# Performance work log

Hardware: AMD Instinct MI355X
Metric: run time of the kernel (lower is better)

## Reference

```python
import jax, jax.numpy as jnp
import numpy as np

B, T, D, H = 32, 512, 512, 8
DH = D // H
NEG = -(2.0 ** 32) + 1.0  # matches torch's (-2**32 + 1) padding value
EPS = 1e-8


def setup_inputs() -> dict:
    key = jax.random.key(0)
    ks = jax.random.split(key, 10)
    s = 1.0 / np.sqrt(D)
    return {
        "queries": jax.random.normal(ks[0], (B, T, D), jnp.float32),
        "keys": jax.random.normal(ks[1], (B, T, D), jnp.float32),
        "Wq": jax.random.normal(ks[2], (D, D), jnp.float32) * s,
        "bq": jnp.zeros((D,), jnp.float32),
        "Wk": jax.random.normal(ks[3], (D, D), jnp.float32) * s,
        "bk": jnp.zeros((D,), jnp.float32),
        "Wv": jax.random.normal(ks[4], (D, D), jnp.float32) * s,
        "bv": jnp.zeros((D,), jnp.float32),
        "gamma": jnp.ones((D,), jnp.float32),
        "beta": jnp.zeros((D,), jnp.float32),
    }


def reference(queries, keys, Wq, bq, Wk, bk, Wv, bv, gamma, beta):
    b, tq, d = queries.shape
    tk = keys.shape[1]
    # projections (torch Linear: x @ W.T + b)
    Q = (queries @ Wq.T + bq).reshape(b, tq, H, DH)
    K = (keys @ Wk.T + bk).reshape(b, tk, H, DH)
    V = (keys @ Wv.T + bv).reshape(b, tk, H, DH)
    # scaled scores: [b, h, tq, tk]
    scores = jnp.einsum("bqhd,bkhd->bhqk", Q, K) / np.float32(np.sqrt(DH))
    # key padding mask (1 where key row sum != 0)
    key_mask = jnp.sign(jnp.abs(keys.sum(-1)))  # [b, tk]
    scores = jnp.where(key_mask[:, None, None, :] == 0, NEG, scores)
    # causal mask
    tril = jnp.tril(jnp.ones((tq, tk), scores.dtype))
    scores = jnp.where(tril[None, None, :, :] == 0, NEG, scores)
    attn = jax.nn.softmax(scores, axis=-1)  # [b, h, tq, tk]
    # query padding mask (zeros out rows for padded queries)
    query_mask = jnp.sign(jnp.abs(queries.sum(-1)))  # [b, tq]
    attn_m = attn * query_mask[:, None, :, None]
    # (dropout_rate == 0 -> identity)
    out = jnp.einsum("bhqk,bkhd->bqhd", attn_m, V).reshape(b, tq, d)
    # residual + LayerNorm (torch .std() is unbiased, ddof=1; eps added to std)
    x = out + queries
    mean = x.mean(-1, keepdims=True)
    std = jnp.std(x, axis=-1, ddof=1, keepdims=True)
    y = gamma * (x - mean) / (std + EPS) + beta
    return y
```

## Files before the change

### kernel.cpp

```cpp
#include <hip/hip_runtime.h>
#include <hip/hip_bf16.h>
#include <math.h>

#define B 32
#define T 512
#define D 512
#define H 8
#define DH 64
#define NEGV (-4294967295.0f)
#define LN_EPS 1e-8f

typedef __attribute__((ext_vector_type(8))) short bf16x8;
typedef __attribute__((ext_vector_type(4))) float f32x4;

__device__ inline f32x4 mfma16(bf16x8 a, bf16x8 b, f32x4 c) {
    return __builtin_amdgcn_mfma_f32_16x16x32_bf16(a, b, c, 0, 0, 0);
}

__device__ inline float fexp2(float x) { return __builtin_amdgcn_exp2f(x); }

#define GLDS16(g, l)                                                      \
    __builtin_amdgcn_global_load_lds(                                     \
        (const __attribute__((address_space(1))) void*)(g),               \
        (__attribute__((address_space(3))) void*)(l), 16, 0, 0)

__device__ inline unsigned short bf16bits(float x) {
    __hip_bfloat16 h = __float2bfloat16(x);
    union { __hip_bfloat16 h; unsigned short u; } cv;
    cv.h = h;
    return cv.u;
}

__global__ __launch_bounds__(256) void convert_mask(
    const float* __restrict__ queries, const float* __restrict__ keys,
    __hip_bfloat16* __restrict__ Qx, __hip_bfloat16* __restrict__ Kx,
    float* __restrict__ qmask, float* __restrict__ kmask)
{
    const int tid = threadIdx.x;
    const int wid = tid >> 6;
    const int lane = tid & 63;
    const int row = blockIdx.x * 4 + wid;
    const float* src = blockIdx.y ? keys : queries;
    __hip_bfloat16* dst = blockIdx.y ? Kx : Qx;
    float* dm = blockIdx.y ? kmask : qmask;

    const float4* p = (const float4*)(src + (size_t)row * 512);
    float4 a = p[lane * 2];
    float4 c = p[lane * 2 + 1];
    float s = a.x + a.y + a.z + a.w + c.x + c.y + c.z + c.w;

    union { unsigned short u[8]; bf16x8 v; } pk;
    pk.u[0] = bf16bits(a.x); pk.u[1] = bf16bits(a.y);
    pk.u[2] = bf16bits(a.z); pk.u[3] = bf16bits(a.w);
    pk.u[4] = bf16bits(c.x); pk.u[5] = bf16bits(c.y);
    pk.u[6] = bf16bits(c.z); pk.u[7] = bf16bits(c.w);
    *(bf16x8*)&dst[(size_t)row * 512 + lane * 8] = pk.v;

#pragma unroll
    for (int off = 32; off > 0; off >>= 1) s += __shfl_xor(s, off, 64);
    if (lane == 0) dm[row] = (s != 0.0f) ? 1.0f : 0.0f;
}

__global__ __launch_bounds__(256) void convert_w(
    const float* __restrict__ Wq, const float* __restrict__ Wk,
    const float* __restrict__ Wv, __hip_bfloat16* __restrict__ Wbf)
{
    const int mat = blockIdx.y;
    const float* Ws = (mat == 0) ? Wq : (mat == 1) ? Wk : Wv;
    const int i = (blockIdx.x * 256 + threadIdx.x) * 8;
    float4 a = *(const float4*)&Ws[i];
    float4 c = *(const float4*)&Ws[i + 4];
    union { unsigned short u[8]; bf16x8 v; } pk;
    pk.u[0] = bf16bits(a.x); pk.u[1] = bf16bits(a.y);
    pk.u[2] = bf16bits(a.z); pk.u[3] = bf16bits(a.w);
    pk.u[4] = bf16bits(c.x); pk.u[5] = bf16bits(c.y);
    pk.u[6] = bf16bits(c.z); pk.u[7] = bf16bits(c.w);
    *(bf16x8*)&Wbf[(size_t)mat * 262144 + i] = pk.v;
}

__global__ __launch_bounds__(256) void qkv_qk(
    const __hip_bfloat16* __restrict__ Qx, const __hip_bfloat16* __restrict__ Kx,
    const __hip_bfloat16* __restrict__ Wbf,
    const float* __restrict__ bq, const float* __restrict__ bk,
    __hip_bfloat16* __restrict__ Qbf, __hip_bfloat16* __restrict__ Kbf)
{
    const int mat = blockIdx.z;
    const __hip_bfloat16* X  = mat ? Kx : Qx;
    const __hip_bfloat16* Wm = Wbf + (size_t)mat * 262144;
    const float* bias = mat ? bk : bq;
    __hip_bfloat16* Out = mat ? Kbf : Qbf;
    const float sc = mat ? 1.0f : 0.18033688011112042f;

    const int bm = blockIdx.x * 128;
    const int bn = blockIdx.y * 128;
    const int tid = threadIdx.x;
    const int w = tid >> 6, lane = tid & 63;
    const int lo = lane & 15, hi = lane >> 4;
    const int wm = (w >> 1) * 64, wn = (w & 1) * 64;

    __shared__ __hip_bfloat16 As[2][128 * 32];
    __shared__ __hip_bfloat16 Bs[2][128 * 32];

    const int r0 = tid >> 2,          g0 = (tid & 3) ^ ((r0 >> 1) & 3);
    const int r1 = (tid + 256) >> 2,  g1 = ((tid + 256) & 3) ^ ((r1 >> 1) & 3);
    const __hip_bfloat16* sA0 = X  + (size_t)(bm + r0) * 512 + g0 * 8;
    const __hip_bfloat16* sA1 = X  + (size_t)(bm + r1) * 512 + g1 * 8;
    const __hip_bfloat16* sB0 = Wm + (size_t)(bn + r0) * 512 + g0 * 8;
    const __hip_bfloat16* sB1 = Wm + (size_t)(bn + r1) * 512 + g1 * 8;
    const int dst0 = (w * 64) * 8;
    const int dst1 = (256 + w * 64) * 8;

    int offA[4], offB[4];
#pragma unroll
    for (int mi = 0; mi < 4; ++mi) {
        int r = wm + mi * 16 + lo;
        offA[mi] = r * 32 + ((hi ^ ((r >> 1) & 3)) * 8);
    }
#pragma unroll
    for (int ni = 0; ni < 4; ++ni) {
        int r = wn + ni * 16 + lo;
        offB[ni] = r * 32 + ((hi ^ ((r >> 1) & 3)) * 8);
    }

    f32x4 acc[4][4];
#pragma unroll
    for (int mi = 0; mi < 4; ++mi)
#pragma unroll
        for (int ni = 0; ni < 4; ++ni)
            acc[mi][ni] = (f32x4){0.f, 0.f, 0.f, 0.f};

    GLDS16(sA0, &As[0][dst0]);
    GLDS16(sA1, &As[0][dst1]);
    GLDS16(sB0, &Bs[0][dst0]);
    GLDS16(sB1, &Bs[0][dst1]);
    __syncthreads();

    for (int kt = 0; kt < 16; ++kt) {
        const int cur = kt & 1;
        if (kt < 15) {
            const int k0 = (kt + 1) * 32;
            GLDS16(sA0 + k0, &As[cur ^ 1][dst0]);
            GLDS16(sA1 + k0, &As[cur ^ 1][dst1]);
            GLDS16(sB0 + k0, &Bs[cur ^ 1][dst0]);
            GLDS16(sB1 + k0, &Bs[cur ^ 1][dst1]);
        }
        bf16x8 af[4], bfr[4];
#pragma unroll
        for (int mi = 0; mi < 4; ++mi) af[mi]  = *(const bf16x8*)&As[cur][offA[mi]];
#pragma unroll
        for (int ni = 0; ni < 4; ++ni) bfr[ni] = *(const bf16x8*)&Bs[cur][offB[ni]];
#pragma unroll
        for (int mi = 0; mi < 4; ++mi)
#pragma unroll
            for (int ni = 0; ni < 4; ++ni)
                acc[mi][ni] = mfma16(bfr[ni], af[mi], acc[mi][ni]);
        __syncthreads();
    }

    float4 b4[4];
#pragma unroll
    for (int ni = 0; ni < 4; ++ni)
        b4[ni] = *(const float4*)&bias[bn + wn + ni * 16 + hi * 4];
#pragma unroll
    for (int mi = 0; mi < 4; ++mi) {
        const size_t tok = bm + wm + mi * 16 + lo;
        __hip_bfloat16* orow = Out + tok * 512 + bn + wn + hi * 4;
#pragma unroll
        for (int ni = 0; ni < 4; ++ni) {
            union { ushort4 u4; unsigned short us[4]; } pk;
            pk.us[0] = bf16bits((acc[mi][ni][0] + b4[ni].x) * sc);
            pk.us[1] = bf16bits((acc[mi][ni][1] + b4[ni].y) * sc);
            pk.us[2] = bf16bits((acc[mi][ni][2] + b4[ni].z) * sc);
            pk.us[3] = bf16bits((acc[mi][ni][3] + b4[ni].w) * sc);
            *(ushort4*)(orow + ni * 16) = pk.u4;
        }
    }
}

__global__ __launch_bounds__(256) void qkv_v(
    const __hip_bfloat16* __restrict__ Kx, const __hip_bfloat16* __restrict__ Wbf,
    const float* __restrict__ bv, __hip_bfloat16* __restrict__ Vtb)
{
    const __hip_bfloat16* X  = Kx;
    const __hip_bfloat16* Wm = Wbf + (size_t)2 * 262144;
    const float* bias = bv;

    const int bm = blockIdx.x * 128;
    const int bn = blockIdx.y * 128;
    const int tid = threadIdx.x;
    const int w = tid >> 6, lane = tid & 63;
    const int lo = lane & 15, hi = lane >> 4;
    const int wm = (w >> 1) * 64, wn = (w & 1) * 64;

    __shared__ __hip_bfloat16 As[2][128 * 32];
    __shared__ __hip_bfloat16 Bs[2][128 * 32];

    const int r0 = tid >> 2,          g0 = (tid & 3) ^ ((r0 >> 1) & 3);
    const int r1 = (tid + 256) >> 2,  g1 = ((tid + 256) & 3) ^ ((r1 >> 1) & 3);
    const __hip_bfloat16* sA0 = X  + (size_t)(bm + r0) * 512 + g0 * 8;
    const __hip_bfloat16* sA1 = X  + (size_t)(bm + r1) * 512 + g1 * 8;
    const __hip_bfloat16* sB0 = Wm + (size_t)(bn + r0) * 512 + g0 * 8;
    const __hip_bfloat16* sB1 = Wm + (size_t)(bn + r1) * 512 + g1 * 8;
    const int dst0 = (w * 64) * 8;
    const int dst1 = (256 + w * 64) * 8;

    int offA[4], offB[4];
#pragma unroll
    for (int mi = 0; mi < 4; ++mi) {
        int r = wm + mi * 16 + lo;
        offA[mi] = r * 32 + ((hi ^ ((r >> 1) & 3)) * 8);
    }
#pragma unroll
    for (int ni = 0; ni < 4; ++ni) {
        int r = wn + ni * 16 + lo;
        offB[ni] = r * 32 + ((hi ^ ((r >> 1) & 3)) * 8);
    }

    f32x4 acc[4][4];
#pragma unroll
    for (int mi = 0; mi < 4; ++mi)
#pragma unroll
        for (int ni = 0; ni < 4; ++ni)
            acc[mi][ni] = (f32x4){0.f, 0.f, 0.f, 0.f};

    GLDS16(sA0, &As[0][dst0]);
    GLDS16(sA1, &As[0][dst1]);
    GLDS16(sB0, &Bs[0][dst0]);
    GLDS16(sB1, &Bs[0][dst1]);
    __syncthreads();

    for (int kt = 0; kt < 16; ++kt) {
        const int cur = kt & 1;
        if (kt < 15) {
            const int k0 = (kt + 1) * 32;
            GLDS16(sA0 + k0, &As[cur ^ 1][dst0]);
            GLDS16(sA1 + k0, &As[cur ^ 1][dst1]);
            GLDS16(sB0 + k0, &Bs[cur ^ 1][dst0]);
            GLDS16(sB1 + k0, &Bs[cur ^ 1][dst1]);
        }
        bf16x8 af[4], bfr[4];
#pragma unroll
        for (int mi = 0; mi < 4; ++mi) af[mi]  = *(const bf16x8*)&As[cur][offA[mi]];
#pragma unroll
        for (int ni = 0; ni < 4; ++ni) bfr[ni] = *(const bf16x8*)&Bs[cur][offB[ni]];
#pragma unroll
        for (int mi = 0; mi < 4; ++mi)
#pragma unroll
            for (int ni = 0; ni < 4; ++ni)
                acc[mi][ni] = mfma16(af[mi], bfr[ni], acc[mi][ni]);
        __syncthreads();
    }

    float bcol[4];
#pragma unroll
    for (int ni = 0; ni < 4; ++ni) bcol[ni] = bias[bn + wn + ni * 16 + lo];
    const int bb = bm >> 9;
    const int tb = (bm & 511) + wm;
#pragma unroll
    for (int ni = 0; ni < 4; ++ni) {
        const int n = bn + wn + ni * 16 + lo;
        const int hh = n >> 6, dh = n & 63;
#pragma unroll
        for (int mi = 0; mi < 4; ++mi) {
            const int tok = tb + mi * 16 + hi * 4;
            const int ktl = tok >> 6, tl = tok & 63;
            union { ushort4 u4; unsigned short us[4]; } pk;
#pragma unroll
            for (int j = 0; j < 4; ++j)
                pk.us[j] = bf16bits(acc[mi][ni][j] + bcol[ni]);
            *(ushort4*)(Vtb + ((((size_t)(bb * 8 + hh) * 8 + ktl) * 64 + dh) * 64 + tl))
                = pk.u4;
        }
    }
}

__global__ __launch_bounds__(256, 4) void flash_attn(
    const __hip_bfloat16* __restrict__ Qbf, const __hip_bfloat16* __restrict__ Kbf,
    const __hip_bfloat16* __restrict__ Vtb, const float* __restrict__ qmask,
    const float* __restrict__ kmask, __hip_bfloat16* __restrict__ Oattn)
{
    const int flat = blockIdx.x + (blockIdx.y << 2) + (blockIdx.z << 5);
    const int rm = ((flat & 7) << 7) + (flat >> 3);
    const int pr = rm & 3;
    const int h  = (rm >> 2) & 7;
    const int b  = rm >> 5;

    const int tid  = threadIdx.x;
    const int w    = tid >> 6;
    const int lane = tid & 63;
    const int lo = lane & 15;
    const int hi = lane >> 4;

    __shared__ __hip_bfloat16 Ks[2][4096];
    __shared__ __hip_bfloat16 p_lds[4][16][72];

    const float* km = kmask + b * T;
    const __hip_bfloat16* Kh = Kbf + (size_t)b * T * D + h * DH;
    const __hip_bfloat16* Vh = Vtb + (size_t)(b * H + h) * T * DH;

    const int sr0 = tid >> 3,         ss0 = tid & 7,        sg0 = ss0 ^ (sr0 & 7);
    const int sr1 = (tid + 256) >> 3, ss1 = (tid + 256) & 7, sg1 = ss1 ^ (sr1 & 7);
    const __hip_bfloat16* sK0 = Kh + (size_t)sr0 * 512 + sg0 * 8;
    const __hip_bfloat16* sK1 = Kh + (size_t)sr1 * 512 + sg1 * 8;
    __hip_bfloat16* dK0a = &Ks[0][w * 512];
    __hip_bfloat16* dK0b = &Ks[0][2048 + w * 512];
    __hip_bfloat16* dK1a = &Ks[1][w * 512];
    __hip_bfloat16* dK1b = &Ks[1][2048 + w * 512];

#define STAGEK(bufp, kt) do {                                              \
        const size_t _o = (size_t)(kt) * 32768;                            \
        GLDS16(sK0 + _o, (bufp) ? dK1a : dK0a);                            \
        GLDS16(sK1 + _o, (bufp) ? dK1b : dK0b);                            \
    } while (0)

    int kfoff[4][2];
#pragma unroll
    for (int c = 0; c < 4; ++c)
#pragma unroll
        for (int j = 0; j < 2; ++j)
            kfoff[c][j] = (c * 16 + lo) * 64 + (((j * 4 + hi) ^ (lo & 7)) * 8);

    const int nt1 = pr + 1;

    int qtile = pr;
    int q = qtile * 64 + w * 16 + lo;
    const __hip_bfloat16* Qrow = Qbf + (size_t)(b * T + q) * D + h * DH;
    bf16x8 qf0 = *(const bf16x8*)(Qrow + hi * 8);
    bf16x8 qf1 = *(const bf16x8*)(Qrow + 32 + hi * 8);

    f32x4 o[4];
    float mrun = -INFINITY, lrun = 0.f;
#pragma unroll
    for (int d = 0; d < 4; ++d) o[d] = (f32x4){0.f, 0.f, 0.f, 0.f};

    STAGEK(0, 0);

    for (int i = 0; i < 9; ++i) {
        const int cur = i & 1;
        if (i < 8) {
            const int nxt = (i + 1 < nt1) ? (i + 1) : (i + 1 - nt1);
            STAGEK(cur ^ 1, nxt);
            asm volatile("s_waitcnt vmcnt(2)" ::: "memory");
        } else {
            asm volatile("s_waitcnt vmcnt(0)" ::: "memory");
        }
        __builtin_amdgcn_s_barrier();
        __builtin_amdgcn_sched_barrier(0);

        if (i == nt1) {
            const float inv = qmask[b * T + q] / lrun;
            __hip_bfloat16* orow = Oattn + (size_t)(b * T + q) * D + h * DH;
#pragma unroll
            for (int db = 0; db < 4; ++db) {
                union { ushort4 u4; unsigned short us[4]; } pk;
#pragma unroll
                for (int j = 0; j < 4; ++j)
                    pk.us[j] = bf16bits(o[db][j] * inv);
                *(ushort4*)(orow + db * 16 + hi * 4) = pk.u4;
            }
            qtile = 7 - pr;
            q = qtile * 64 + w * 16 + lo;
            const __hip_bfloat16* Qrow2 = Qbf + (size_t)(b * T + q) * D + h * DH;
            qf0 = *(const bf16x8*)(Qrow2 + hi * 8);
            qf1 = *(const bf16x8*)(Qrow2 + 32 + hi * 8);
            mrun = -INFINITY; lrun = 0.f;
#pragma unroll
            for (int d = 0; d < 4; ++d) o[d] = (f32x4){0.f, 0.f, 0.f, 0.f};
        }

        const int kt = (i < nt1) ? i : (i - nt1);
        const int kb = kt * 64;

        const __hip_bfloat16* Vtile = Vh + (size_t)kt * 4096;
        bf16x8 vf[4][2];
#pragma unroll
        for (int db = 0; db < 4; ++db) {
            const __hip_bfloat16* Vrow = Vtile + (db * 16 + lo) * 64;
            vf[db][0] = *(const bf16x8*)(Vrow + hi * 8);
            vf[db][1] = *(const bf16x8*)(Vrow + 32 + hi * 8);
        }

        bf16x8 kf[4][2];
#pragma unroll
        for (int c = 0; c < 4; ++c) {
            kf[c][0] = *(const bf16x8*)&Ks[cur][kfoff[c][0]];
            kf[c][1] = *(const bf16x8*)&Ks[cur][kfoff[c][1]];
        }

        f32x4 S[4];
#pragma unroll
        for (int c = 0; c < 4; ++c) {
            f32x4 acc = (f32x4){0.f, 0.f, 0.f, 0.f};
            acc = mfma16(kf[c][0], qf0, acc);
            acc = mfma16(kf[c][1], qf1, acc);
            const float4 kmv = *(const float4*)(km + kb + c * 16 + hi * 4);
            const float kmj[4] = {kmv.x, kmv.y, kmv.z, kmv.w};
#pragma unroll
            for (int j = 0; j < 4; ++j) {
                const int key = kb + c * 16 + hi * 4 + j;
                acc[j] = (key <= q && kmj[j] != 0.0f) ? acc[j] : NEGV;
            }
            S[c] = acc;
        }

        float tm0 = fmaxf(fmaxf(S[0][0], S[0][1]), fmaxf(S[0][2], S[0][3]));
        float tm1 = fmaxf(fmaxf(S[1][0], S[1][1]), fmaxf(S[1][2], S[1][3]));
        float tm2 = fmaxf(fmaxf(S[2][0], S[2][1]), fmaxf(S[2][2], S[2][3]));
        float tm3 = fmaxf(fmaxf(S[3][0], S[3][1]), fmaxf(S[3][2], S[3][3]));
        float tm = fmaxf(fmaxf(tm0, tm1), fmaxf(tm2, tm3));
        tm = fmaxf(tm, __shfl_xor(tm, 16, 64));
        tm = fmaxf(tm, __shfl_xor(tm, 32, 64));

        const float nm = fmaxf(mrun, tm);
        const float alpha = fexp2(mrun - nm);
        mrun = nm;
#pragma unroll
        for (int d = 0; d < 4; ++d)
#pragma unroll
            for (int j = 0; j < 4; ++j)
                o[d][j] *= alpha;

        float ps = 0.f;
#pragma unroll
        for (int c = 0; c < 4; ++c) {
            union { ushort4 u4; unsigned short us[4]; } pk;
#pragma unroll
            for (int j = 0; j < 4; ++j) {
                float p = fexp2(S[c][j] - nm);
                ps += p;
                pk.us[j] = bf16bits(p);
            }
            *(ushort4*)&p_lds[w][lo][c * 16 + hi * 4] = pk.u4;
        }
        ps += __shfl_xor(ps, 16, 64);
        ps += __shfl_xor(ps, 32, 64);
        lrun = lrun * alpha + ps;

        asm volatile("s_waitcnt lgkmcnt(0)" ::: "memory");
        __builtin_amdgcn_sched_barrier(0);

#pragma unroll
        for (int half = 0; half < 2; ++half) {
            bf16x8 pf = *(const bf16x8*)&p_lds[w][lo][half * 32 + hi * 8];
#pragma unroll
            for (int db = 0; db < 4; ++db)
                o[db] = mfma16(vf[db][half], pf, o[db]);
        }

        __builtin_amdgcn_s_barrier();
    }

    {
        const float inv = qmask[b * T + q] / lrun;
        __hip_bfloat16* orow = Oattn + (size_t)(b * T + q) * D + h * DH;
#pragma unroll
        for (int db = 0; db < 4; ++db) {
            union { ushort4 u4; unsigned short us[4]; } pk;
#pragma unroll
            for (int j = 0; j < 4; ++j)
                pk.us[j] = bf16bits(o[db][j] * inv);
            *(ushort4*)(orow + db * 16 + hi * 4) = pk.u4;
        }
    }
#undef STAGEK
}

__device__ inline float wave_sum(float v) {
#pragma unroll
    for (int off = 32; off > 0; off >>= 1) v += __shfl_xor(v, off, 64);
    return v;
}

__global__ __launch_bounds__(256) void resid_ln(
    const __hip_bfloat16* __restrict__ Oa, const float* __restrict__ queries,
    const float* __restrict__ gamma, const float* __restrict__ beta,
    float* __restrict__ out)
{
    const int row = blockIdx.x;
    const int tid = threadIdx.x;
    const int wid = tid >> 6;
    const int lane = tid & 63;
    __shared__ float red[4];

    const size_t base = (size_t)row * 512;
    float2 qv = *(const float2*)&queries[base + 2 * tid];
    unsigned ov = *(const unsigned*)((const unsigned short*)Oa + base + 2 * tid);
    union { unsigned u; float f; } c0, c1;
    c0.u = ov << 16;
    c1.u = ov & 0xffff0000u;
    float x0 = c0.f + qv.x;
    float x1 = c1.f + qv.y;

    float part = wave_sum(x0 + x1);
    if (lane == 0) red[wid] = part;
    __syncthreads();
    float mean = (red[0] + red[1] + red[2] + red[3]) * (1.0f / 512.0f);
    __syncthreads();

    float d0 = x0 - mean, d1 = x1 - mean;
    part = wave_sum(d0 * d0 + d1 * d1);
    if (lane == 0) red[wid] = part;
    __syncthreads();
    float var = (red[0] + red[1] + red[2] + red[3]) * (1.0f / 511.0f);
    float denom = sqrtf(var) + LN_EPS;

    float2 g = *(const float2*)&gamma[2 * tid];
    float2 be = *(const float2*)&beta[2 * tid];
    float2 res;
    res.x = g.x * d0 / denom + be.x;
    res.y = g.y * d1 / denom + be.y;
    *(float2*)&out[base + 2 * tid] = res;
}

extern "C" void kernel_launch(void* const* d_in, const int* in_sizes, int n_in,
                              void* d_out, int out_size, void* d_ws, size_t ws_size,
                              hipStream_t stream)
{
    const float* queries = (const float*)d_in[0];
    const float* keys    = (const float*)d_in[1];
    const float* Wq      = (const float*)d_in[2];
    const float* bq      = (const float*)d_in[3];
    const float* Wk      = (const float*)d_in[4];
    const float* bk      = (const float*)d_in[5];
    const float* Wv      = (const float*)d_in[6];
    const float* bv      = (const float*)d_in[7];
    const float* gamma   = (const float*)d_in[8];
    const float* beta    = (const float*)d_in[9];
    float* out = (float*)d_out;

    char* ws = (char*)d_ws;
    __hip_bfloat16* Qbf   = (__hip_bfloat16*)(ws);
    __hip_bfloat16* Kbf   = (__hip_bfloat16*)(ws + 16777216);
    __hip_bfloat16* Vtb   = (__hip_bfloat16*)(ws + 33554432);
    __hip_bfloat16* Qx    = (__hip_bfloat16*)(ws + 50331648);
    __hip_bfloat16* Oattn = (__hip_bfloat16*)(ws + 50331648);
    __hip_bfloat16* Kx    = (__hip_bfloat16*)(ws + 67108864);
    __hip_bfloat16* Wbf   = (__hip_bfloat16*)(ws + 83886080);
    float* qmask          = (float*)(ws + 85458944);
    float* kmask          = (float*)(ws + 85524480);

    convert_mask<<<dim3(4096, 2), 256, 0, stream>>>(
        queries, keys, Qx, Kx, qmask, kmask);
    convert_w<<<dim3(128, 3), 256, 0, stream>>>(Wq, Wk, Wv, Wbf);
    qkv_qk<<<dim3(128, 4, 2), 256, 0, stream>>>(
        Qx, Kx, Wbf, bq, bk, Qbf, Kbf);
    qkv_v<<<dim3(128, 4), 256, 0, stream>>>(Kx, Wbf, bv, Vtb);
    flash_attn<<<dim3(4, 8, 32), 256, 0, stream>>>(
        Qbf, Kbf, Vtb, qmask, kmask, Oattn);
    resid_ln<<<16384, 256, 0, stream>>>(Oattn, queries, gamma, beta, out);
}
```

Baseline: 134.4 us.

## Triple-buffer K tiles, prefetch V and masks, use additive mask biases

```diff
diff --git a/kernel.cpp b/kernel.cpp
--- a/kernel.cpp
+++ b/kernel.cpp
@@ -58,7 +58,9 @@
 
 #pragma unroll
     for (int off = 32; off > 0; off >>= 1) s += __shfl_xor(s, off, 64);
-    if (lane == 0) dm[row] = (s != 0.0f) ? 1.0f : 0.0f;
+    if (lane == 0)
+        dm[row] = blockIdx.y ? ((s != 0.0f) ? 0.0f : NEGV)
+                             : ((s != 0.0f) ? 1.0f : 0.0f);
 }
 
 __global__ __launch_bounds__(256) void convert_w(
@@ -277,7 +279,7 @@
 __global__ __launch_bounds__(256, 4) void flash_attn(
     const __hip_bfloat16* __restrict__ Qbf, const __hip_bfloat16* __restrict__ Kbf,
     const __hip_bfloat16* __restrict__ Vtb, const float* __restrict__ qmask,
-    const float* __restrict__ kmask, __hip_bfloat16* __restrict__ Oattn)
+    const float* __restrict__ kmneg, __hip_bfloat16* __restrict__ Oattn)
 {
     const int flat = blockIdx.x + (blockIdx.y << 2) + (blockIdx.z << 5);
     const int rm = ((flat & 7) << 7) + (flat >> 3);
@@ -285,32 +287,26 @@
     const int h  = (rm >> 2) & 7;
     const int b  = rm >> 5;
 
-    const int tid  = threadIdx.x;
-    const int w    = tid >> 6;
-    const int lane = tid & 63;
-    const int lo = lane & 15;
-    const int hi = lane >> 4;
-
-    __shared__ __hip_bfloat16 Ks[2][4096];
+    const int tid = threadIdx.x;
+    const int w = tid >> 6, lane = tid & 63;
+    const int lo = lane & 15, hi = lane >> 4;
+
+    __shared__ __hip_bfloat16 Ks[3][4096];
     __shared__ __hip_bfloat16 p_lds[4][16][72];
 
-    const float* km = kmask + b * T;
+    const float* km = kmneg + b * T;
     const __hip_bfloat16* Kh = Kbf + (size_t)b * T * D + h * DH;
     const __hip_bfloat16* Vh = Vtb + (size_t)(b * H + h) * T * DH;
 
-    const int sr0 = tid >> 3,         ss0 = tid & 7,        sg0 = ss0 ^ (sr0 & 7);
-    const int sr1 = (tid + 256) >> 3, ss1 = (tid + 256) & 7, sg1 = ss1 ^ (sr1 & 7);
+    const int sr0 = tid >> 3,         sg0 = (tid & 7) ^ (sr0 & 7);
+    const int sr1 = (tid + 256) >> 3, sg1 = ((tid + 256) & 7) ^ (sr1 & 7);
     const __hip_bfloat16* sK0 = Kh + (size_t)sr0 * 512 + sg0 * 8;
     const __hip_bfloat16* sK1 = Kh + (size_t)sr1 * 512 + sg1 * 8;
-    __hip_bfloat16* dK0a = &Ks[0][w * 512];
-    __hip_bfloat16* dK0b = &Ks[0][2048 + w * 512];
-    __hip_bfloat16* dK1a = &Ks[1][w * 512];
-    __hip_bfloat16* dK1b = &Ks[1][2048 + w * 512];
-
-#define STAGEK(bufp, kt) do {                                              \
+
+#define STAGEK(buf, kt) do {                                               \
         const size_t _o = (size_t)(kt) * 32768;                            \
-        GLDS16(sK0 + _o, (bufp) ? dK1a : dK0a);                            \
-        GLDS16(sK1 + _o, (bufp) ? dK1b : dK0b);                            \
+        GLDS16(sK0 + _o, &Ks[buf][w * 512]);                               \
+        GLDS16(sK1 + _o, &Ks[buf][2048 + w * 512]);                        \
     } while (0)
 
     int kfoff[4][2];
@@ -320,13 +316,26 @@
         for (int j = 0; j < 2; ++j)
             kfoff[c][j] = (c * 16 + lo) * 64 + (((j * 4 + hi) ^ (lo & 7)) * 8);
 
+    f32x4 cb[4];
+#pragma unroll
+    for (int c = 0; c < 4; ++c)
+#pragma unroll
+        for (int j = 0; j < 4; ++j)
+            cb[c][j] = (c * 16 + hi * 4 + j <= w * 16 + lo) ? 0.0f : NEGV;
+
     const int nt1 = pr + 1;
-
-    int qtile = pr;
-    int q = qtile * 64 + w * 16 + lo;
-    const __hip_bfloat16* Qrow = Qbf + (size_t)(b * T + q) * D + h * DH;
-    bf16x8 qf0 = *(const bf16x8*)(Qrow + hi * 8);
-    bf16x8 qf1 = *(const bf16x8*)(Qrow + 32 + hi * 8);
+    const int qA = pr * 64 + w * 16 + lo;
+    const int qB = (7 - pr) * 64 + w * 16 + lo;
+
+    const __hip_bfloat16* QrA = Qbf + (size_t)(b * T + qA) * D + h * DH;
+    const __hip_bfloat16* QrB = Qbf + (size_t)(b * T + qB) * D + h * DH;
+    const bf16x8 qfA0 = *(const bf16x8*)(QrA + hi * 8);
+    const bf16x8 qfA1 = *(const bf16x8*)(QrA + 32 + hi * 8);
+    const bf16x8 qfB0 = *(const bf16x8*)(QrB + hi * 8);
+    const bf16x8 qfB1 = *(const bf16x8*)(QrB + 32 + hi * 8);
+
+    int q = qA;
+    bf16x8 qf0 = qfA0, qf1 = qfA1;
 
     f32x4 o[4];
     float mrun = -INFINITY, lrun = 0.f;
@@ -335,14 +344,32 @@
 
     STAGEK(0, 0);
 
+    int bcur = 0;
     for (int i = 0; i < 9; ++i) {
-        const int cur = i & 1;
+        const int kt = (i < nt1) ? i : (i - nt1);
+        const int kb = kt * 64;
+        const bool diag = (i == nt1 - 1) || (i == 8);
+
+        const __hip_bfloat16* Vtile = Vh + (size_t)kt * 4096;
+        bf16x8 vf[4][2];
+#pragma unroll
+        for (int db = 0; db < 4; ++db) {
+            const __hip_bfloat16* Vrow = Vtile + (db * 16 + lo) * 64;
+            vf[db][0] = *(const bf16x8*)(Vrow + hi * 8);
+            vf[db][1] = *(const bf16x8*)(Vrow + 32 + hi * 8);
+        }
+        f32x4 kmb[4];
+#pragma unroll
+        for (int c = 0; c < 4; ++c)
+            kmb[c] = *(const f32x4*)(km + kb + c * 16 + hi * 4);
+
+        const int bnext = (bcur == 2) ? 0 : bcur + 1;
         if (i < 8) {
-            const int nxt = (i + 1 < nt1) ? (i + 1) : (i + 1 - nt1);
-            STAGEK(cur ^ 1, nxt);
-            asm volatile("s_waitcnt vmcnt(2)" ::: "memory");
+            const int nkt = (i + 1 < nt1) ? (i + 1) : (i + 1 - nt1);
+            STAGEK(bnext, nkt);
+            asm volatile("s_waitcnt vmcnt(14)" ::: "memory");
         } else {
-            asm volatile("s_waitcnt vmcnt(0)" ::: "memory");
+            asm volatile("s_waitcnt vmcnt(12)" ::: "memory");
         }
         __builtin_amdgcn_s_barrier();
         __builtin_amdgcn_sched_barrier(0);
@@ -358,33 +385,17 @@
                     pk.us[j] = bf16bits(o[db][j] * inv);
                 *(ushort4*)(orow + db * 16 + hi * 4) = pk.u4;
             }
-            qtile = 7 - pr;
-            q = qtile * 64 + w * 16 + lo;
-            const __hip_bfloat16* Qrow2 = Qbf + (size_t)(b * T + q) * D + h * DH;
-            qf0 = *(const bf16x8*)(Qrow2 + hi * 8);
-            qf1 = *(const bf16x8*)(Qrow2 + 32 + hi * 8);
+            q = qB; qf0 = qfB0; qf1 = qfB1;
             mrun = -INFINITY; lrun = 0.f;
 #pragma unroll
             for (int d = 0; d < 4; ++d) o[d] = (f32x4){0.f, 0.f, 0.f, 0.f};
         }
 
-        const int kt = (i < nt1) ? i : (i - nt1);
-        const int kb = kt * 64;
-
-        const __hip_bfloat16* Vtile = Vh + (size_t)kt * 4096;
-        bf16x8 vf[4][2];
-#pragma unroll
-        for (int db = 0; db < 4; ++db) {
-            const __hip_bfloat16* Vrow = Vtile + (db * 16 + lo) * 64;
-            vf[db][0] = *(const bf16x8*)(Vrow + hi * 8);
-            vf[db][1] = *(const bf16x8*)(Vrow + 32 + hi * 8);
-        }
-
         bf16x8 kf[4][2];
 #pragma unroll
         for (int c = 0; c < 4; ++c) {
-            kf[c][0] = *(const bf16x8*)&Ks[cur][kfoff[c][0]];
-            kf[c][1] = *(const bf16x8*)&Ks[cur][kfoff[c][1]];
+            kf[c][0] = *(const bf16x8*)&Ks[bcur][kfoff[c][0]];
+            kf[c][1] = *(const bf16x8*)&Ks[bcur][kfoff[c][1]];
         }
 
         f32x4 S[4];
@@ -393,13 +404,8 @@
             f32x4 acc = (f32x4){0.f, 0.f, 0.f, 0.f};
             acc = mfma16(kf[c][0], qf0, acc);
             acc = mfma16(kf[c][1], qf1, acc);
-            const float4 kmv = *(const float4*)(km + kb + c * 16 + hi * 4);
-            const float kmj[4] = {kmv.x, kmv.y, kmv.z, kmv.w};
-#pragma unroll
-            for (int j = 0; j < 4; ++j) {
-                const int key = kb + c * 16 + hi * 4 + j;
-                acc[j] = (key <= q && kmj[j] != 0.0f) ? acc[j] : NEGV;
-            }
+            acc += kmb[c];
+            if (diag) acc += cb[c];
             S[c] = acc;
         }
 
@@ -446,8 +452,7 @@
             for (int db = 0; db < 4; ++db)
                 o[db] = mfma16(vf[db][half], pf, o[db]);
         }
-
-        __builtin_amdgcn_s_barrier();
+        bcur = bnext;
     }
 
     {
```

Result: slower. 151.6 us (+12.7%).
